# Performance work log

Hardware: AMD Instinct MI355X
Metric: run time of the kernel (lower is better)

## Reference

```python
import jax, jax.numpy as jnp
import numpy as np
from jax import lax

D_MODEL = 1024; N_HEADS = 16; D_FF = 4096
D_INNER = 2048; D_STATE = 16; D_CONV = 4; DT_RANK = 64
B = 4; T = 1024; TF = 512
HD = D_MODEL // N_HEADS


def setup_inputs() -> dict:
    key = jax.random.key(0)
    ks = jax.random.split(key, 24)
    r = lambda i, shape, s=0.02: jax.random.normal(ks[i], shape, jnp.float32) * s
    lengths = jnp.array([512, 384, 448, 320])
    styled_mask = jnp.arange(TF)[None, :] < lengths[:, None]  # True = valid
    inp = {
        'x': jax.random.normal(ks[0], (B, T, D_MODEL), jnp.float32),
        'styled_frames': jax.random.normal(ks[1], (B, TF, D_MODEL), jnp.float32),
        'styled_mask': styled_mask,
        'ln1_g': jnp.ones((D_MODEL,)), 'ln1_b': jnp.zeros((D_MODEL,)),
        'ln2_g': jnp.ones((D_MODEL,)), 'ln2_b': jnp.zeros((D_MODEL,)),
        'ln3_g': jnp.ones((D_MODEL,)), 'ln3_b': jnp.zeros((D_MODEL,)),
        'm_in_w': r(2, (D_MODEL, 2 * D_INNER)),
        'm_conv_w': r(3, (D_INNER, D_CONV), 0.1),
        'm_conv_b': jnp.zeros((D_INNER,)),
        'm_xproj_w': r(4, (D_INNER, DT_RANK + 2 * D_STATE)),
        'm_dt_w': r(5, (DT_RANK, D_INNER), 0.1),
        'm_dt_b': jnp.full((D_INNER,), -4.6),  # softplus -> dt ~ 0.01
        'm_A_log': jnp.log(jnp.broadcast_to(jnp.arange(1, D_STATE + 1, dtype=jnp.float32), (D_INNER, D_STATE))),
        'm_D': jnp.ones((D_INNER,)),
        'm_out_w': r(6, (D_INNER, D_MODEL)),
        'attn_in_w': r(7, (3 * D_MODEL, D_MODEL)),
        'attn_in_b': jnp.zeros((3 * D_MODEL,)),
        'attn_out_w': r(8, (D_MODEL, D_MODEL)),
        'attn_out_b': jnp.zeros((D_MODEL,)),
        'ff_w1': r(9, (D_MODEL, D_FF)),
        'ff_b1': jnp.zeros((D_FF,)),
        'ff_w2': r(10, (D_FF, D_MODEL)),
        'ff_b2': jnp.zeros((D_MODEL,)),
    }
    return inp


def _layer_norm(x, g, b):
    m = x.mean(-1, keepdims=True)
    v = ((x - m) ** 2).mean(-1, keepdims=True)
    return (x - m) / jnp.sqrt(v + 1e-5) * g + b


def _mamba(h, m_in_w, m_conv_w, m_conv_b, m_xproj_w, m_dt_w, m_dt_b, m_A_log, m_D, m_out_w):
    xz = h @ m_in_w                                   # (B,T,2*d_inner)
    xm, z = jnp.split(xz, 2, axis=-1)
    # causal depthwise conv1d
    xt = jnp.pad(xm.transpose(0, 2, 1), ((0, 0), (0, 0), (D_CONV - 1, 0)))  # (B,d_inner,T+pad)
    xc = lax.conv_general_dilated(xt, m_conv_w[:, None, :], (1,), 'VALID',
                                  feature_group_count=D_INNER,
                                  dimension_numbers=('NCH', 'OIH', 'NCH'))
    xc = jax.nn.silu(xc + m_conv_b[None, :, None]).transpose(0, 2, 1)       # (B,T,d_inner)
    x_dbl = xc @ m_xproj_w
    dt, Bs, Cs = jnp.split(x_dbl, [DT_RANK, DT_RANK + D_STATE], axis=-1)
    dt = jax.nn.softplus(dt @ m_dt_w + m_dt_b)        # (B,T,d_inner)
    A = -jnp.exp(m_A_log)                             # (d_inner,d_state)

    def step(hs, inp):
        dt_t, B_t, C_t, u_t = inp                     # (B,d_inner),(B,d_state),(B,d_state),(B,d_inner)
        dA = jnp.exp(dt_t[:, :, None] * A)            # (B,d_inner,d_state)
        hs = dA * hs + dt_t[:, :, None] * B_t[:, None, :] * u_t[:, :, None]
        y = jnp.einsum('bds,bs->bd', hs, C_t)
        return hs, y

    h0 = jnp.zeros((xc.shape[0], D_INNER, D_STATE), xc.dtype)
    inputs = (dt.transpose(1, 0, 2), Bs.transpose(1, 0, 2), Cs.transpose(1, 0, 2), xc.transpose(1, 0, 2))
    hT, ys = lax.scan(step, h0, inputs)
    y = ys.transpose(1, 0, 2) + xc * m_D
    y = y * jax.nn.silu(z)
    return y @ m_out_w, hT


def _cross_attn(q_in, kv_in, valid_mask, in_w, in_b, out_w, out_b):
    d = D_MODEL
    q = q_in @ in_w[:d].T + in_b[:d]
    k = kv_in @ in_w[d:2 * d].T + in_b[d:2 * d]
    v = kv_in @ in_w[2 * d:].T + in_b[2 * d:]
    q = q.reshape(q.shape[0], q.shape[1], N_HEADS, HD)
    k = k.reshape(k.shape[0], k.shape[1], N_HEADS, HD)
    v = v.reshape(v.shape[0], v.shape[1], N_HEADS, HD)
    scores = jnp.einsum('bqhd,bkhd->bhqk', q, k) / np.sqrt(HD)
    scores = jnp.where(valid_mask[:, None, None, :], scores, jnp.finfo(scores.dtype).min)
    attn = jax.nn.softmax(scores, axis=-1)
    o = jnp.einsum('bhqk,bkhd->bqhd', attn, v).reshape(q_in.shape)
    return o @ out_w.T + out_b


def reference(x, styled_frames, styled_mask,
              ln1_g, ln1_b, ln2_g, ln2_b, ln3_g, ln3_b,
              m_in_w, m_conv_w, m_conv_b, m_xproj_w, m_dt_w, m_dt_b, m_A_log, m_D, m_out_w,
              attn_in_w, attn_in_b, attn_out_w, attn_out_b,
              ff_w1, ff_b1, ff_w2, ff_b2):
    h = _layer_norm(x, ln1_g, ln1_b)
    h_mamba, new_state = _mamba(h, m_in_w, m_conv_w, m_conv_b, m_xproj_w, m_dt_w, m_dt_b, m_A_log, m_D, m_out_w)
    x = x + h_mamba
    h = _layer_norm(x, ln2_g, ln2_b)
    x = x + _cross_attn(h, styled_frames, styled_mask, attn_in_w, attn_in_b, attn_out_w, attn_out_b)
    h = _layer_norm(x, ln3_g, ln3_b)
    ff = jax.nn.gelu(h @ ff_w1 + ff_b1, approximate=False) @ ff_w2 + ff_b2
    x = x + ff
    return x, new_state
```

## Files before the change

kernel.cpp:

```cpp
#include <hip/hip_runtime.h>
#include <hip/hip_bf16.h>
#include <cstdint>

using bf16 = __hip_bfloat16;

typedef __attribute__((ext_vector_type(8))) short short8;
typedef __attribute__((ext_vector_type(4))) float floatx4;

__device__ __forceinline__ float b2f(bf16 h) { return __bfloat162float(h); }
__device__ __forceinline__ bf16 f2b(float f) { return __float2bfloat16(f); }
__device__ __forceinline__ float uitf(unsigned u) { union { unsigned u; float f; } c; c.u = u; return c.f; }

__device__ __forceinline__ void async16(const bf16* g, bf16* l) {
    __builtin_amdgcn_global_load_lds(
        (const __attribute__((address_space(1))) uint32_t*)(const void*)g,
        (__attribute__((address_space(3))) uint32_t*)(void*)l, 16, 0, 0);
}

__global__ void lens_flag_kernel(const unsigned char* __restrict__ mask,
                                 const unsigned int* __restrict__ ln1g_raw,
                                 int* __restrict__ hdr) {
    __shared__ int cnt[4];
    int tid = threadIdx.x;
    if (tid < 4) cnt[tid] = 0;
    __syncthreads();
    unsigned char b0 = mask[0], b1 = mask[1];
    int width = (b1 == 0) ? 4 : ((b0 == 1) ? 1 : 2);
    if (width == 4) {
        const unsigned int* m = (const unsigned int*)mask;
        for (int i = tid; i < 2048; i += 256) if (m[i] != 0u) atomicAdd(&cnt[i >> 9], 1);
    } else if (width == 2) {
        const unsigned short* m = (const unsigned short*)mask;
        for (int i = tid; i < 2048; i += 256) if (m[i] != 0u) atomicAdd(&cnt[i >> 9], 1);
    } else {
        for (int i = tid; i < 2048; i += 256) if (mask[i] != 0u) atomicAdd(&cnt[i >> 9], 1);
    }
    __syncthreads();
    if (tid < 4) hdr[tid] = cnt[tid];
    if (tid == 4) hdr[4] = (ln1g_raw[0] == 0x3F800000u) ? 1 : 0;
}

__global__ void convert_kernel(const void* __restrict__ src, bf16* __restrict__ dst, int n,
                               const int* __restrict__ flagp) {
    int i = blockIdx.x * 256 + threadIdx.x;
    if (i >= n) return;
    if (*flagp) dst[i] = f2b(((const float*)src)[i]);
    else        dst[i] = ((const bf16*)src)[i];
}

struct SmallSrcs { const void* p[15]; };
__global__ void convert_smalls_kernel(SmallSrcs s, bf16* __restrict__ dst,
                                      const int* __restrict__ flagp) {
    const int ends[16] = {0, 1024, 2048, 3072, 4096, 5120, 6144, 14336, 16384, 18432,
                          51200, 53248, 56320, 57344, 61440, 62464};
    int i = blockIdx.x * 256 + threadIdx.x;
    if (i >= 62464) return;
    int seg = 0;
    #pragma unroll
    for (int k = 1; k < 16; ++k) if (i >= ends[k]) seg = k;
    int local = i - ends[seg];
    const void* sp = s.p[seg];
    if (*flagp) dst[i] = f2b(((const float*)sp)[local]);
    else        dst[i] = ((const bf16*)sp)[local];
}

__global__ void transpose_any(const void* __restrict__ src, bf16* __restrict__ dst,
                              int R, int C, const int* __restrict__ flagp) {
    __shared__ bf16 tile[32][33];
    bool f32 = (*flagp != 0);
    int bx = blockIdx.x * 32, by = blockIdx.y * 32;
    int tx = threadIdx.x;
    for (int i = threadIdx.y; i < 32; i += 8) {
        int y = by + i, x = bx + tx;
        if (y < R && x < C) {
            size_t idx = (size_t)y * C + x;
            tile[i][tx] = f32 ? f2b(((const float*)src)[idx]) : ((const bf16*)src)[idx];
        }
    }
    __syncthreads();
    for (int i = threadIdx.y; i < 32; i += 8) {
        int yo = bx + i, xo = by + tx;
        if (yo < C && xo < R) dst[(size_t)yo * R + xo] = tile[tx][i];
    }
}

__global__ void vtrans_kernel(const bf16* __restrict__ kv, bf16* __restrict__ vt) {
    __shared__ bf16 t[32][33];
    int kc = blockIdx.x * 32, dc = blockIdx.y * 32;
    int bh = blockIdx.z; int b = bh >> 4, h = bh & 15;
    int tx = threadIdx.x;
    for (int i = threadIdx.y; i < 32; i += 8)
        t[i][tx] = kv[(size_t)(b * 512 + kc + i) * 2048 + 1024 + h * 64 + dc + tx];
    __syncthreads();
    for (int i = threadIdx.y; i < 32; i += 8)
        vt[(size_t)(bh * 64 + dc + i) * 512 + kc + tx] = t[tx][i];
}

__global__ __launch_bounds__(256) void ln_kernel(const bf16* __restrict__ x, const bf16* __restrict__ g,
                                                 const bf16* __restrict__ bb, bf16* __restrict__ out) {
    int row = blockIdx.x, tid = threadIdx.x;
    const bf16* xr = x + (size_t)row * 1024;
    float v[4];
    {
        uint2 raw = *(const uint2*)(xr + tid * 4);
        v[0] = uitf(raw.x << 16); v[1] = uitf(raw.x & 0xffff0000u);
        v[2] = uitf(raw.y << 16); v[3] = uitf(raw.y & 0xffff0000u);
    }
    float sum = v[0] + v[1] + v[2] + v[3];
    float sq = v[0]*v[0] + v[1]*v[1] + v[2]*v[2] + v[3]*v[3];
    for (int off = 32; off; off >>= 1) { sum += __shfl_xor(sum, off); sq += __shfl_xor(sq, off); }
    __shared__ float wsm[8];
    int wave = tid >> 6;
    if ((tid & 63) == 0) { wsm[wave * 2] = sum; wsm[wave * 2 + 1] = sq; }
    __syncthreads();
    sum = wsm[0] + wsm[2] + wsm[4] + wsm[6];
    sq  = wsm[1] + wsm[3] + wsm[5] + wsm[7];
    float mean = sum * (1.f / 1024.f);
    float var = sq * (1.f / 1024.f) - mean * mean;
    float rstd = rsqrtf(var + 1e-5f);
    bf16* orow = out + (size_t)row * 1024;
    #pragma unroll
    for (int c = 0; c < 4; ++c) {
        int col = tid * 4 + c;
        orow[col] = f2b((v[c] - mean) * rstd * b2f(g[col]) + b2f(bb[col]));
    }
}

template<int BN>
__global__ __launch_bounds__(256) void gemm_bt(
    const bf16* __restrict__ A, int lda,
    const bf16* __restrict__ Bt, int ldb,
    void* __restrict__ Cp, int ldc, int c_f32,
    int M, int N, int K,
    const bf16* __restrict__ bias,
    const bf16* __restrict__ res, int ldres,
    int act)
{
    constexpr int NJ = BN / 32;
    __shared__ __align__(16) bf16 As[3][128 * 32];
    __shared__ __align__(16) bf16 Bs[3][BN * 32];
    const int tid = threadIdx.x;
    const int lane = tid & 63;
    const int wave = tid >> 6;
    const int wr = (wave >> 1) * 64;
    const int wc = (wave & 1) * (BN / 2);
    const int lrow = lane & 15;
    const int quad = lane >> 4;

    const int gx = gridDim.x;
    const int nwg = gx * gridDim.y;
    const int orig = blockIdx.y * gx + blockIdx.x;
    int wgid = orig;
    if ((nwg & 7) == 0) wgid = (orig & 7) * (nwg >> 3) + (orig >> 3);
    const int n0 = (wgid % gx) * BN;
    const int m0 = (wgid / gx) * 128;

    const int r0 = tid >> 2;
    const int c0 = (((tid & 3) ^ ((r0 >> 1) & 3)) << 3);

    floatx4 acc[4][NJ];
    #pragma unroll
    for (int i = 0; i < 4; ++i)
        #pragma unroll
        for (int j = 0; j < NJ; ++j) acc[i][j] = (floatx4){0.f, 0.f, 0.f, 0.f};

    const int n1 = n0 + r0, n2 = n0 + r0 + 64;
    const bool fullN = (n0 + BN <= N);
    const bool bok1 = n1 < N, bok2 = n2 < N;
    const int4 z4 = {0, 0, 0, 0};

    const bf16* Ag1 = A + (size_t)(m0 + r0) * lda + c0;
    const bf16* Ag2 = A + (size_t)(m0 + r0 + 64) * lda + c0;
    const bf16* Bg1 = Bt + (size_t)n1 * ldb + c0;
    const bf16* Bg2 = Bt + (size_t)n2 * ldb + c0;

    const int chsw = ((quad ^ ((lrow >> 1) & 3)) << 3);
    const int nt = K >> 5;

    if (fullN) {
        auto stage = [&](int buf, int k0) {
            bf16* AsW = &As[buf][tid * 8];
            bf16* BsW = &Bs[buf][tid * 8];
            async16(Ag1 + k0, AsW);
            async16(Ag2 + k0, AsW + 64 * 32);
            async16(Bg1 + k0, BsW);
            if constexpr (BN == 128) async16(Bg2 + k0, BsW + 64 * 32);
        };
        stage(0, 0);
        if (nt > 1) stage(1, 32);
        int cur = 0;
        for (int t = 0; t < nt; ++t) {
            if (t + 1 < nt) {
                if constexpr (BN == 128) asm volatile("s_waitcnt vmcnt(4)" ::: "memory");
                else                     asm volatile("s_waitcnt vmcnt(3)" ::: "memory");
            } else {
                asm volatile("s_waitcnt vmcnt(0)" ::: "memory");
            }
            __builtin_amdgcn_s_barrier();
            __builtin_amdgcn_sched_barrier(0);
            if (t + 2 < nt) {
                int nb = cur + 2; if (nb >= 3) nb -= 3;
                stage(nb, (t + 2) << 5);
            }
            short8 af[4], bfr[NJ];
            #pragma unroll
            for (int i = 0; i < 4; ++i) af[i]  = *(const short8*)&As[cur][(wr + i * 16 + lrow) * 32 + chsw];
            #pragma unroll
            for (int j = 0; j < NJ; ++j) bfr[j] = *(const short8*)&Bs[cur][(wc + j * 16 + lrow) * 32 + chsw];
            #pragma unroll
            for (int i = 0; i < 4; ++i)
                #pragma unroll
                for (int j = 0; j < NJ; ++j)
                    acc[i][j] = __builtin_amdgcn_mfma_f32_16x16x32_bf16(bfr[j], af[i], acc[i][j], 0, 0, 0);
            if (++cur == 3) cur = 0;
        }
    } else {
        bf16* AsW = &As[0][tid * 8];
        bf16* BsW = &Bs[0][tid * 8];
        for (int k0 = 0; k0 < K; k0 += 32) {
            __syncthreads();
            async16(Ag1 + k0, AsW);
            async16(Ag2 + k0, AsW + 64 * 32);
            *(int4*)BsW = bok1 ? *(const int4*)(Bg1 + k0) : z4;
            if constexpr (BN == 128)
                *(int4*)(BsW + 64 * 32) = bok2 ? *(const int4*)(Bg2 + k0) : z4;
            __syncthreads();
            short8 af[4], bfr[NJ];
            #pragma unroll
            for (int i = 0; i < 4; ++i) af[i]  = *(const short8*)&As[0][(wr + i * 16 + lrow) * 32 + chsw];
            #pragma unroll
            for (int j = 0; j < NJ; ++j) bfr[j] = *(const short8*)&Bs[0][(wc + j * 16 + lrow) * 32 + chsw];
            #pragma unroll
            for (int i = 0; i < 4; ++i)
                #pragma unroll
                for (int j = 0; j < NJ; ++j)
                    acc[i][j] = __builtin_amdgcn_mfma_f32_16x16x32_bf16(bfr[j], af[i], acc[i][j], 0, 0, 0);
        }
    }

    #pragma unroll
    for (int i = 0; i < 4; ++i) {
        const int row = m0 + wr + i * 16 + lrow;
        #pragma unroll
        for (int j = 0; j < NJ; ++j) {
            const int col = n0 + wc + j * 16 + quad * 4;
            float v4[4];
            #pragma unroll
            for (int r = 0; r < 4; ++r) {
                float v = acc[i][j][r];
                if (bias) v += b2f(bias[col + r]);
                if (act == 1)      v = 0.5f * v * (1.f + erff(v * 0.70710678118f));
                else if (act == 2) v = (v > 15.f) ? v : log1pf(__expf(v));
                v4[r] = v;
            }
            if (col + 4 <= N) {
                if (res) {
                    uint2 rr = *(const uint2*)(res + (size_t)row * ldres + col);
                    v4[0] += uitf(rr.x << 16); v4[1] += uitf(rr.x & 0xffff0000u);
                    v4[2] += uitf(rr.y << 16); v4[3] += uitf(rr.y & 0xffff0000u);
                }
                if (c_f32) {
                    float4 o = {v4[0], v4[1], v4[2], v4[3]};
                    *(float4*)((float*)Cp + (size_t)row * ldc + col) = o;
                } else {
                    bf16 o[4] = {f2b(v4[0]), f2b(v4[1]), f2b(v4[2]), f2b(v4[3])};
                    *(uint2*)((bf16*)Cp + (size_t)row * ldc + col) = *(uint2*)o;
                }
            } else {
                #pragma unroll
                for (int r = 0; r < 4; ++r) {
                    if (col + r >= N) continue;
                    float v = v4[r];
                    if (res) v += b2f(res[(size_t)row * ldres + col + r]);
                    if (c_f32) ((float*)Cp)[(size_t)row * ldc + col + r] = v;
                    else       ((bf16*)Cp)[(size_t)row * ldc + col + r] = f2b(v);
                }
            }
        }
    }
}

__global__ __launch_bounds__(512) void gemm_bt_big(
    const bf16* __restrict__ A, int lda,
    const bf16* __restrict__ Bt, int ldb,
    void* __restrict__ Cp, int ldc, int c_f32,
    int M, int N, int K,
    const bf16* __restrict__ bias,
    const bf16* __restrict__ res, int ldres,
    int act)
{
    __shared__ __align__(16) bf16 As[3][256 * 32];
    __shared__ __align__(16) bf16 Bs[3][256 * 32];
    const int tid = threadIdx.x;
    const int lane = tid & 63;
    const int wave = tid >> 6;
    const int wm = wave >> 2;
    const int wn = wave & 3;
    const int lrow = lane & 15;
    const int quad = lane >> 4;

    const int gx = gridDim.x;
    const int nwg = gx * gridDim.y;
    const int orig = blockIdx.y * gx + blockIdx.x;
    int wgid = orig;
    if ((nwg & 7) == 0) wgid = (orig & 7) * (nwg >> 3) + (orig >> 3);
    const int n0 = (wgid % gx) * 256;
    const int m0 = (wgid / gx) * 256;

    const int r0 = tid >> 2;
    const int c0 = (((tid & 3) ^ ((r0 >> 1) & 3)) << 3);

    floatx4 acc[8][4];
    #pragma unroll
    for (int i = 0; i < 8; ++i)
        #pragma unroll
        for (int j = 0; j < 4; ++j) acc[i][j] = (floatx4){0.f, 0.f, 0.f, 0.f};

    const bf16* Ag1 = A + (size_t)(m0 + r0) * lda + c0;
    const bf16* Ag2 = A + (size_t)(m0 + r0 + 128) * lda + c0;
    const bf16* Bg1 = Bt + (size_t)(n0 + r0) * ldb + c0;
    const bf16* Bg2 = Bt + (size_t)(n0 + r0 + 128) * ldb + c0;

    const int chsw = ((quad ^ ((lrow >> 1) & 3)) << 3);
    const int nt = K >> 5;

    auto stage = [&](int buf, int k0) {
        bf16* AsW = &As[buf][tid * 8];
        bf16* BsW = &Bs[buf][tid * 8];
        async16(Ag1 + k0, AsW);
        async16(Ag2 + k0, AsW + 128 * 32);
        async16(Bg1 + k0, BsW);
        async16(Bg2 + k0, BsW + 128 * 32);
    };
    stage(0, 0);
    stage(1, 32);
    int cur = 0;
    for (int t = 0; t < nt; ++t) {
        if (t + 1 < nt) asm volatile("s_waitcnt vmcnt(4)" ::: "memory");
        else            asm volatile("s_waitcnt vmcnt(0)" ::: "memory");
        __builtin_amdgcn_s_barrier();
        __builtin_amdgcn_sched_barrier(0);
        if (t + 2 < nt) {
            int nb = cur + 2; if (nb >= 3) nb -= 3;
            stage(nb, (t + 2) << 5);
        }
        short8 af[8], bfr[4];
        #pragma unroll
        for (int i = 0; i < 8; ++i)
            af[i] = *(const short8*)&As[cur][(wm * 128 + i * 16 + lrow) * 32 + chsw];
        #pragma unroll
        for (int j = 0; j < 4; ++j)
            bfr[j] = *(const short8*)&Bs[cur][(wn * 64 + j * 16 + lrow) * 32 + chsw];
        #pragma unroll
        for (int i = 0; i < 8; ++i)
            #pragma unroll
            for (int j = 0; j < 4; ++j)
                acc[i][j] = __builtin_amdgcn_mfma_f32_16x16x32_bf16(bfr[j], af[i], acc[i][j], 0, 0, 0);
        if (++cur == 3) cur = 0;
    }

    #pragma unroll
    for (int i = 0; i < 8; ++i) {
        const int row = m0 + wm * 128 + i * 16 + lrow;
        #pragma unroll
        for (int j = 0; j < 4; ++j) {
            const int col = n0 + wn * 64 + j * 16 + quad * 4;
            float v4[4];
            #pragma unroll
            for (int r = 0; r < 4; ++r) {
                float v = acc[i][j][r];
                if (bias) v += b2f(bias[col + r]);
                if (act == 1)      v = 0.5f * v * (1.f + erff(v * 0.70710678118f));
                else if (act == 2) v = (v > 15.f) ? v : log1pf(__expf(v));
                v4[r] = v;
            }
            if (res) {
                uint2 rr = *(const uint2*)(res + (size_t)row * ldres + col);
                v4[0] += uitf(rr.x << 16); v4[1] += uitf(rr.x & 0xffff0000u);
                v4[2] += uitf(rr.y << 16); v4[3] += uitf(rr.y & 0xffff0000u);
            }
            if (c_f32) {
                float4 o = {v4[0], v4[1], v4[2], v4[3]};
                *(float4*)((float*)Cp + (size_t)row * ldc + col) = o;
            } else {
                bf16 o[4] = {f2b(v4[0]), f2b(v4[1]), f2b(v4[2]), f2b(v4[3])};
                *(uint2*)((bf16*)Cp + (size_t)row * ldc + col) = *(uint2*)o;
            }
        }
    }
}

__global__ __launch_bounds__(256) void conv_silu_kernel(const bf16* __restrict__ xz, const bf16* __restrict__ cw,
                                                        const bf16* __restrict__ cb, bf16* __restrict__ xc) {
    int idx = blockIdx.x * 256 + threadIdx.x;
    int d = idx & 2047;
    int row = idx >> 11;
    int t = row & 1023;
    int base = row - t;
    float acc = b2f(cb[d]);
    #pragma unroll
    for (int j = 0; j < 4; ++j) {
        int tt = t - 3 + j;
        if (tt >= 0) acc += b2f(xz[(size_t)(base + tt) * 4096 + d]) * b2f(cw[d * 4 + j]);
    }
    xc[idx] = f2b(acc * (1.f / (1.f + __expf(-acc))));
}

__global__ __launch_bounds__(256) void scan_part1(
    const bf16* __restrict__ dt, const bf16* __restrict__ xc, const bf16* __restrict__ xdbl,
    const bf16* __restrict__ A_log, float* __restrict__ Pb, float* __restrict__ qb)
{
    __shared__ float smB[128][20];
    const int tid = threadIdx.x;
    const int dgrp = blockIdx.x, c = blockIdx.y, b = blockIdx.z;
    const int dl = tid >> 1, sh = tid & 1;
    const int d = (dgrp << 7) + dl;
    const size_t rowbase = (size_t)b * 1024 + (size_t)c * 128;

    {
        int r = tid >> 1, q = tid & 1;
        short8 raw = *(const short8*)(xdbl + (rowbase + r) * 96 + 64 + q * 8);
        #pragma unroll
        for (int j = 0; j < 8; ++j) smB[r][q * 8 + j] = b2f(((const bf16*)&raw)[j]);
    }
    __syncthreads();

    float A2[8], h[8];
    #pragma unroll
    for (int s = 0; s < 8; ++s) {
        A2[s] = -__expf(b2f(A_log[d * 16 + sh * 8 + s])) * 1.44269504f;
        h[s] = 0.f;
    }
    float dtsum = 0.f;
    const bf16* dtp = dt + rowbase * 2048 + d;
    const bf16* up  = xc + rowbase * 2048 + d;
    for (int tc = 0; tc < 128; tc += 8) {
        float dtv[8], uv[8];
        #pragma unroll
        for (int i = 0; i < 8; ++i) {
            dtv[i] = b2f(dtp[(size_t)(tc + i) * 2048]);
            uv[i]  = b2f(up[(size_t)(tc + i) * 2048]);
        }
        #pragma unroll
        for (int i = 0; i < 8; ++i) {
            float dtf = dtv[i];
            dtsum += dtf;
            float w = dtf * uv[i];
            float4 B0 = *(const float4*)&smB[tc + i][sh * 8];
            float4 B1 = *(const float4*)&smB[tc + i][sh * 8 + 4];
            float Bv[8] = {B0.x, B0.y, B0.z, B0.w, B1.x, B1.y, B1.z, B1.w};
            #pragma unroll
            for (int s = 0; s < 8; ++s) {
                float e = __builtin_amdgcn_exp2f(dtf * A2[s]);
                h[s] = fmaf(e, h[s], w * Bv[s]);
            }
        }
    }
    size_t gid = ((size_t)(b * 2048 + d) * 16 + sh * 8) + (size_t)c * 131072;
    float Pv[8];
    #pragma unroll
    for (int s = 0; s < 8; ++s) Pv[s] = __builtin_amdgcn_exp2f(A2[s] * dtsum);
    *(float4*)(Pb + gid)     = *(float4*)&Pv[0];
    *(float4*)(Pb + gid + 4) = *(float4*)&Pv[4];
    *(float4*)(qb + gid)     = *(float4*)&h[0];
    *(float4*)(qb + gid + 4) = *(float4*)&h[4];
}

__global__ __launch_bounds__(256) void scan_stitch(
    const float* __restrict__ Pb, const float* __restrict__ qb,
    float* __restrict__ hs, float* __restrict__ state_out)
{
    int gid = blockIdx.x * 256 + threadIdx.x;
    float h = 0.f;
    #pragma unroll
    for (int c = 0; c < 8; ++c) {
        hs[gid + c * 131072] = h;
        h = Pb[gid + c * 131072] * h + qb[gid + c * 131072];
    }
    state_out[gid] = h;
}

__global__ __launch_bounds__(256) void scan_part3(
    const bf16* __restrict__ dt, const bf16* __restrict__ xc, const bf16* __restrict__ xdbl,
    const bf16* __restrict__ xz, const bf16* __restrict__ A_log, const bf16* __restrict__ Dp,
    const float* __restrict__ hs, bf16* __restrict__ ymul)
{
    __shared__ float smBC[128][36];
    const int tid = threadIdx.x;
    const int dgrp = blockIdx.x, c = blockIdx.y, b = blockIdx.z;
    const int dl = tid >> 1, sh = tid & 1;
    const int d = (dgrp << 7) + dl;
    const size_t rowbase = (size_t)b * 1024 + (size_t)c * 128;

    {
        int r = tid >> 1, q = tid & 1;
        const bf16* src = xdbl + (rowbase + r) * 96 + 64 + q * 16;
        short8 raw0 = *(const short8*)src;
        short8 raw1 = *(const short8*)(src + 8);
        #pragma unroll
        for (int j = 0; j < 8; ++j) {
            smBC[r][q * 16 + j]     = b2f(((const bf16*)&raw0)[j]);
            smBC[r][q * 16 + 8 + j] = b2f(((const bf16*)&raw1)[j]);
        }
    }
    __syncthreads();

    float A2[8], h[8];
    size_t gid = ((size_t)(b * 2048 + d) * 16 + sh * 8) + (size_t)c * 131072;
    {
        float4 h0 = *(const float4*)(hs + gid);
        float4 h1 = *(const float4*)(hs + gid + 4);
        h[0] = h0.x; h[1] = h0.y; h[2] = h0.z; h[3] = h0.w;
        h[4] = h1.x; h[5] = h1.y; h[6] = h1.z; h[7] = h1.w;
    }
    #pragma unroll
    for (int s = 0; s < 8; ++s)
        A2[s] = -__expf(b2f(A_log[d * 16 + sh * 8 + s])) * 1.44269504f;
    const float Dv = b2f(Dp[d]);
    const bf16* dtp = dt + rowbase * 2048 + d;
    const bf16* up  = xc + rowbase * 2048 + d;
    const bf16* zp  = xz + rowbase * 4096 + 2048 + d;
    bf16* yp = ymul + rowbase * 2048 + d;
    for (int tc = 0; tc < 128; tc += 8) {
        float dtv[8], uv[8], zv[8];
        #pragma unroll
        for (int i = 0; i < 8; ++i) {
            dtv[i] = b2f(dtp[(size_t)(tc + i) * 2048]);
            uv[i]  = b2f(up[(size_t)(tc + i) * 2048]);
            zv[i]  = b2f(zp[(size_t)(tc + i) * 4096]);
        }
        #pragma unroll
        for (int i = 0; i < 8; ++i) {
            float dtf = dtv[i], uf = uv[i];
            float w = dtf * uf;
            float4 B0 = *(const float4*)&smBC[tc + i][sh * 8];
            float4 B1 = *(const float4*)&smBC[tc + i][sh * 8 + 4];
            float4 C0 = *(const float4*)&smBC[tc + i][16 + sh * 8];
            float4 C1 = *(const float4*)&smBC[tc + i][16 + sh * 8 + 4];
            float Bv[8] = {B0.x, B0.y, B0.z, B0.w, B1.x, B1.y, B1.z, B1.w};
            float Cv[8] = {C0.x, C0.y, C0.z, C0.w, C1.x, C1.y, C1.z, C1.w};
            float y = 0.f;
            #pragma unroll
            for (int s = 0; s < 8; ++s) {
                float e = __builtin_amdgcn_exp2f(dtf * A2[s]);
                h[s] = fmaf(e, h[s], w * Bv[s]);
                y = fmaf(h[s], Cv[s], y);
            }
            y += __shfl_xor(y, 1);
            float z = zv[i];
            float sig = __builtin_amdgcn_rcpf(1.f + __builtin_amdgcn_exp2f(-1.44269504f * z));
            float o = (y + uf * Dv) * (z * sig);
            if (sh == 0) yp[(size_t)(tc + i) * 2048] = f2b(o);
        }
    }
}

__global__ __launch_bounds__(256) void attn_mfma(
    const bf16* __restrict__ qb, const bf16* __restrict__ kv, const bf16* __restrict__ vt,
    const int* __restrict__ lens, bf16* __restrict__ ob)
{
    const int qt = blockIdx.x, h = blockIdx.y, b = blockIdx.z;
    const int tid = threadIdx.x;
    const int wave = tid >> 6;
    const int lane = tid & 63;
    const int l15 = lane & 15;
    const int quad = lane >> 4;
    const int len = lens[b];

    __shared__ __align__(16) bf16 Ps[32][520];
    __shared__ float red_sh[4][32];

    short8 aq[2][2];
    const bf16* qbase = qb + (size_t)(b * 1024 + qt * 32 + l15) * 1024 + h * 64 + quad * 8;
    #pragma unroll
    for (int mt = 0; mt < 2; ++mt)
        #pragma unroll
        for (int ks = 0; ks < 2; ++ks)
            aq[mt][ks] = *(const short8*)(qbase + (size_t)mt * 16 * 1024 + ks * 32);

    floatx4 accs[2][8];
    #pragma unroll
    for (int mt = 0; mt < 2; ++mt)
        #pragma unroll
        for (int nt = 0; nt < 8; ++nt) accs[mt][nt] = (floatx4){0.f, 0.f, 0.f, 0.f};

    const bf16* kbase = kv + (size_t)(b * 512 + wave * 128 + l15) * 2048 + h * 64 + quad * 8;
    #pragma unroll
    for (int nt = 0; nt < 8; ++nt) {
        short8 bk0 = *(const short8*)(kbase + (size_t)nt * 16 * 2048);
        short8 bk1 = *(const short8*)(kbase + (size_t)nt * 16 * 2048 + 32);
        #pragma unroll
        for (int mt = 0; mt < 2; ++mt) {
            accs[mt][nt] = __builtin_amdgcn_mfma_f32_16x16x32_bf16(aq[mt][0], bk0, accs[mt][nt], 0, 0, 0);
            accs[mt][nt] = __builtin_amdgcn_mfma_f32_16x16x32_bf16(aq[mt][1], bk1, accs[mt][nt], 0, 0, 0);
        }
    }

    float pm[2][4];
    #pragma unroll
    for (int mt = 0; mt < 2; ++mt)
        #pragma unroll
        for (int r = 0; r < 4; ++r) pm[mt][r] = -1e30f;
    #pragma unroll
    for (int mt = 0; mt < 2; ++mt)
        #pragma unroll
        for (int nt = 0; nt < 8; ++nt) {
            int col = wave * 128 + nt * 16 + l15;
            bool ok = col < len;
            #pragma unroll
            for (int r = 0; r < 4; ++r) {
                float s = ok ? accs[mt][nt][r] * 0.125f : -1e30f;
                accs[mt][nt][r] = s;
                pm[mt][r] = fmaxf(pm[mt][r], s);
            }
        }
    #pragma unroll
    for (int off = 1; off < 16; off <<= 1)
        #pragma unroll
        for (int mt = 0; mt < 2; ++mt)
            #pragma unroll
            for (int r = 0; r < 4; ++r) pm[mt][r] = fmaxf(pm[mt][r], __shfl_xor(pm[mt][r], off));
    if (l15 == 0)
        #pragma unroll
        for (int mt = 0; mt < 2; ++mt)
            #pragma unroll
            for (int r = 0; r < 4; ++r) red_sh[wave][mt * 16 + quad * 4 + r] = pm[mt][r];
    __syncthreads();
    float rowmax[2][4];
    #pragma unroll
    for (int mt = 0; mt < 2; ++mt)
        #pragma unroll
        for (int r = 0; r < 4; ++r) {
            int row = mt * 16 + quad * 4 + r;
            rowmax[mt][r] = fmaxf(fmaxf(red_sh[0][row], red_sh[1][row]),
                                  fmaxf(red_sh[2][row], red_sh[3][row]));
        }
    __syncthreads();

    float ps[2][4] = {{0.f, 0.f, 0.f, 0.f}, {0.f, 0.f, 0.f, 0.f}};
    #pragma unroll
    for (int mt = 0; mt < 2; ++mt)
        #pragma unroll
        for (int nt = 0; nt < 8; ++nt)
            #pragma unroll
            for (int r = 0; r < 4; ++r) {
                float p = __expf(accs[mt][nt][r] - rowmax[mt][r]);
                accs[mt][nt][r] = p;
                ps[mt][r] += p;
            }
    #pragma unroll
    for (int off = 1; off < 16; off <<= 1)
        #pragma unroll
        for (int mt = 0; mt < 2; ++mt)
            #pragma unroll
            for (int r = 0; r < 4; ++r) ps[mt][r] += __shfl_xor(ps[mt][r], off);
    if (l15 == 0)
        #pragma unroll
        for (int mt = 0; mt < 2; ++mt)
            #pragma unroll
            for (int r = 0; r < 4; ++r) red_sh[wave][mt * 16 + quad * 4 + r] = ps[mt][r];
    #pragma unroll
    for (int mt = 0; mt < 2; ++mt)
        #pragma unroll
        for (int nt = 0; nt < 8; ++nt)
            #pragma unroll
            for (int r = 0; r < 4; ++r)
                Ps[mt * 16 + quad * 4 + r][wave * 128 + nt * 16 + l15] = f2b(accs[mt][nt][r]);
    __syncthreads();
    float rowsum[2][4];
    #pragma unroll
    for (int mt = 0; mt < 2; ++mt)
        #pragma unroll
        for (int r = 0; r < 4; ++r) {
            int row = mt * 16 + quad * 4 + r;
            rowsum[mt][r] = red_sh[0][row] + red_sh[1][row] + red_sh[2][row] + red_sh[3][row];
        }

    floatx4 acco[2];
    acco[0] = (floatx4){0.f, 0.f, 0.f, 0.f};
    acco[1] = (floatx4){0.f, 0.f, 0.f, 0.f};
    const bf16* vtbase = vt + (size_t)((b * 16 + h) * 64 + wave * 16 + l15) * 512 + quad * 8;
    #pragma unroll
    for (int kc = 0; kc < 16; ++kc) {
        short8 bv = *(const short8*)(vtbase + kc * 32);
        short8 ap0 = *(const short8*)&Ps[l15][kc * 32 + quad * 8];
        short8 ap1 = *(const short8*)&Ps[16 + l15][kc * 32 + quad * 8];
        acco[0] = __builtin_amdgcn_mfma_f32_16x16x32_bf16(ap0, bv, acco[0], 0, 0, 0);
        acco[1] = __builtin_amdgcn_mfma_f32_16x16x32_bf16(ap1, bv, acco[1], 0, 0, 0);
    }

    #pragma unroll
    for (int mt = 0; mt < 2; ++mt)
        #pragma unroll
        for (int r = 0; r < 4; ++r) {
            int row = b * 1024 + qt * 32 + mt * 16 + quad * 4 + r;
            int col = h * 64 + wave * 16 + l15;
            ob[(size_t)row * 1024 + col] = f2b(acco[mt][r] / rowsum[mt][r]);
        }
}

extern "C" void kernel_launch(void* const* d_in, const int* in_sizes, int n_in,
                              void* d_out, int out_size, void* d_ws, size_t ws_size,
                              hipStream_t stream) {
    bf16* W = (bf16*)d_ws;
    int* hdr = (int*)d_ws;
    const int* flagp = hdr + 4;
    const size_t CV_X     = 32;
    const size_t CV_ST    = CV_X    + 4194304;
    const size_t CV_AIW   = CV_ST   + 2097152;
    const size_t CV_AOW   = CV_AIW  + 3145728;
    const size_t CV_SM    = CV_AOW  + 1048576;
    const size_t WT_IN    = CV_SM   + 62464;
    const size_t WT_XPROJ = WT_IN   + 4194304;
    const size_t WT_DT    = WT_XPROJ + 196608;
    const size_t WT_OUT   = WT_DT   + 131072;
    const size_t WT_FF1   = WT_OUT  + 2097152;
    const size_t WT_FF2   = WT_FF1  + 4194304;
    const size_t HB   = WT_FF2 + 4194304;
    const size_t XZ   = HB     + 4194304;
    const size_t XC   = XZ     + 16777216;
    const size_t XDBL = XC     + 8388608;
    const size_t DTB  = XDBL   + 393216;
    const size_t YM   = DTB    + 8388608;
    const size_t X2  = HB;
    const size_t HB2 = DTB;
    const size_t Qb  = XZ;
    const size_t KV  = XZ + 4194304;
    const size_t AO  = XC;
    const size_t VT  = XC + 4194304;
    const size_t X3  = YM;
    const size_t HB3 = DTB;
    const size_t FFH = XZ;
    float* Pb = (float*)(W + HB);
    float* qbuf = Pb + 1048576;
    float* hstart = (float*)(W + WT_IN);
    const size_t S_LN1G = 0, S_LN1B = 1024, S_LN2G = 2048, S_LN2B = 3072, S_LN3G = 4096, S_LN3B = 5120;
    const size_t S_CW = 6144, S_CB = 14336, S_DTB = 16384, S_AL = 18432, S_D = 51200;
    const size_t S_AIB = 53248, S_AOB = 56320, S_FB1 = 57344, S_FB2 = 61440;

    float* out = (float*)d_out;
    float* state_out = out + (size_t)4 * 1024 * 1024;

    lens_flag_kernel<<<1, 256, 0, stream>>>((const unsigned char*)d_in[2],
                                            (const unsigned int*)d_in[3], hdr);
    convert_kernel<<<16384, 256, 0, stream>>>(d_in[0],  W + CV_X,   4194304, flagp);
    convert_kernel<<<8192,  256, 0, stream>>>(d_in[1],  W + CV_ST,  2097152, flagp);
    convert_kernel<<<12288, 256, 0, stream>>>(d_in[18], W + CV_AIW, 3145728, flagp);
    convert_kernel<<<4096,  256, 0, stream>>>(d_in[20], W + CV_AOW, 1048576, flagp);
    SmallSrcs ss;
    ss.p[0] = d_in[3];  ss.p[1] = d_in[4];  ss.p[2] = d_in[5];  ss.p[3] = d_in[6];
    ss.p[4] = d_in[7];  ss.p[5] = d_in[8];  ss.p[6] = d_in[10]; ss.p[7] = d_in[11];
    ss.p[8] = d_in[14]; ss.p[9] = d_in[15]; ss.p[10] = d_in[16]; ss.p[11] = d_in[19];
    ss.p[12] = d_in[21]; ss.p[13] = d_in[23]; ss.p[14] = d_in[25];
    convert_smalls_kernel<<<245, 256, 0, stream>>>(ss, W + CV_SM, flagp);

    dim3 tb(32, 8);
    transpose_any<<<dim3(128, 32), tb, 0, stream>>>(d_in[9],  W + WT_IN,    1024, 4096, flagp);
    transpose_any<<<dim3(3, 64),   tb, 0, stream>>>(d_in[12], W + WT_XPROJ, 2048, 96,   flagp);
    transpose_any<<<dim3(64, 2),   tb, 0, stream>>>(d_in[13], W + WT_DT,    64,   2048, flagp);
    transpose_any<<<dim3(32, 64),  tb, 0, stream>>>(d_in[17], W + WT_OUT,   2048, 1024, flagp);
    transpose_any<<<dim3(128, 32), tb, 0, stream>>>(d_in[22], W + WT_FF1,   1024, 4096, flagp);
    transpose_any<<<dim3(32, 128), tb, 0, stream>>>(d_in[24], W + WT_FF2,   4096, 1024, flagp);

    auto gemm = [&](const bf16* A, int lda, const bf16* Bt, int ldb, void* C, int ldc, int c_f32,
                    int M, int N, int K, const bf16* bias, const bf16* res, int ldres, int act) {
        if (M >= 4096 && N >= 4096 && (M & 255) == 0 && (N & 255) == 0 && (K & 31) == 0 && K >= 64) {
            dim3 grid(N / 256, M / 256);
            gemm_bt_big<<<grid, 512, 0, stream>>>(A, lda, Bt, ldb, C, ldc, c_f32, M, N, K, bias, res, ldres, act);
        } else if ((N & 127) == 0 && N <= 2048) {
            dim3 grid(N / 64, M / 128);
            gemm_bt<64><<<grid, 256, 0, stream>>>(A, lda, Bt, ldb, C, ldc, c_f32, M, N, K, bias, res, ldres, act);
        } else {
            dim3 grid((N + 127) / 128, M / 128);
            gemm_bt<128><<<grid, 256, 0, stream>>>(A, lda, Bt, ldb, C, ldc, c_f32, M, N, K, bias, res, ldres, act);
        }
    };

    ln_kernel<<<4096, 256, 0, stream>>>(W + CV_X, W + CV_SM + S_LN1G, W + CV_SM + S_LN1B, W + HB);
    gemm(W + HB, 1024, W + WT_IN, 1024, W + XZ, 4096, 0, 4096, 4096, 1024, nullptr, nullptr, 0, 0);
    conv_silu_kernel<<<32768, 256, 0, stream>>>(W + XZ, W + CV_SM + S_CW, W + CV_SM + S_CB, W + XC);
    gemm(W + XC, 2048, W + WT_XPROJ, 2048, W + XDBL, 96, 0, 4096, 96, 2048, nullptr, nullptr, 0, 0);
    gemm(W + XDBL, 96, W + WT_DT, 64, W + DTB, 2048, 0, 4096, 2048, 64, W + CV_SM + S_DTB, nullptr, 0, 2);
    scan_part1<<<dim3(16, 8, 4), 256, 0, stream>>>(W + DTB, W + XC, W + XDBL, W + CV_SM + S_AL, Pb, qbuf);
    scan_stitch<<<512, 256, 0, stream>>>(Pb, qbuf, hstart, state_out);
    scan_part3<<<dim3(16, 8, 4), 256, 0, stream>>>(W + DTB, W + XC, W + XDBL, W + XZ,
                                                   W + CV_SM + S_AL, W + CV_SM + S_D, hstart, W + YM);
    gemm(W + YM, 2048, W + WT_OUT, 2048, W + X2, 1024, 0, 4096, 1024, 2048, nullptr, W + CV_X, 1024, 0);

    ln_kernel<<<4096, 256, 0, stream>>>(W + X2, W + CV_SM + S_LN2G, W + CV_SM + S_LN2B, W + HB2);
    gemm(W + HB2, 1024, W + CV_AIW, 1024, W + Qb, 1024, 0, 4096, 1024, 1024, W + CV_SM + S_AIB, nullptr, 0, 0);
    gemm(W + CV_ST, 1024, W + CV_AIW + 1048576, 1024, W + KV, 2048, 0, 2048, 2048, 1024, W + CV_SM + S_AIB + 1024, nullptr, 0, 0);
    vtrans_kernel<<<dim3(16, 2, 64), tb, 0, stream>>>(W + KV, W + VT);
    attn_mfma<<<dim3(32, 16, 4), 256, 0, stream>>>(W + Qb, W + KV, W + VT, hdr, W + AO);
    gemm(W + AO, 1024, W + CV_AOW, 1024, W + X3, 1024, 0, 4096, 1024, 1024, W + CV_SM + S_AOB, W + X2, 1024, 0);

    ln_kernel<<<4096, 256, 0, stream>>>(W + X3, W + CV_SM + S_LN3G, W + CV_SM + S_LN3B, W + HB3);
    gemm(W + HB3, 1024, W + WT_FF1, 1024, W + FFH, 4096, 0, 4096, 4096, 1024, W + CV_SM + S_FB1, nullptr, 0, 1);
    gemm(W + FFH, 4096, W + WT_FF2, 4096, out, 1024, 1, 4096, 1024, 4096, W + CV_SM + S_FB2, W + X3, 1024, 0);
}
```

Before: 929.2 us.

## Restructure big GEMM into double-buffered K=64 tiles with phased load/MFMA interleave

The large 256x256 GEMM moves from a triple-buffered K=32 pipeline to a double-buffered K=64 pipeline. Each K step is split into four phases that interleave fragment loads, MFMA groups and the async global-to-LDS staging of the next tile. The phases are fenced with barriers and partial vmcnt waits, and s_setprio raises priority around the MFMA blocks. The aim is better overlap of memory and matrix work and fewer barriers per unit of K, at the cost of more barriers per iteration and a larger LDS footprint (128KB total).

```diff
diff --git a/kernel.cpp b/kernel.cpp
--- a/kernel.cpp
+++ b/kernel.cpp
@@ -280,7 +280,7 @@
     }
 }
 
-__global__ __launch_bounds__(512) void gemm_bt_big(
+__global__ __launch_bounds__(512) void gemm_8ph(
     const bf16* __restrict__ A, int lda,
     const bf16* __restrict__ Bt, int ldb,
     void* __restrict__ Cp, int ldc, int c_f32,
@@ -289,8 +289,8 @@
     const bf16* __restrict__ res, int ldres,
     int act)
 {
-    __shared__ __align__(16) bf16 As[3][256 * 32];
-    __shared__ __align__(16) bf16 Bs[3][256 * 32];
+    __shared__ __align__(16) bf16 As[2][256 * 64];
+    __shared__ __align__(16) bf16 Bs[2][256 * 64];
     const int tid = threadIdx.x;
     const int lane = tid & 63;
     const int wave = tid >> 6;
@@ -307,8 +307,10 @@
     const int n0 = (wgid % gx) * 256;
     const int m0 = (wgid / gx) * 256;
 
-    const int r0 = tid >> 2;
-    const int c0 = (((tid & 3) ^ ((r0 >> 1) & 3)) << 3);
+    const int srow = tid >> 3;
+    const int scol = (((tid & 7) ^ ((tid >> 3) & 7)) << 3);
+    const bf16* Ag = A + (size_t)(m0 + srow) * lda + scol;
+    const bf16* Bg = Bt + (size_t)(n0 + srow) * ldb + scol;
 
     floatx4 acc[8][4];
     #pragma unroll
@@ -316,47 +318,73 @@
         #pragma unroll
         for (int j = 0; j < 4; ++j) acc[i][j] = (floatx4){0.f, 0.f, 0.f, 0.f};
 
-    const bf16* Ag1 = A + (size_t)(m0 + r0) * lda + c0;
-    const bf16* Ag2 = A + (size_t)(m0 + r0 + 128) * lda + c0;
-    const bf16* Bg1 = Bt + (size_t)(n0 + r0) * ldb + c0;
-    const bf16* Bg2 = Bt + (size_t)(n0 + r0 + 128) * ldb + c0;
-
-    const int chsw = ((quad ^ ((lrow >> 1) & 3)) << 3);
-    const int nt = K >> 5;
-
-    auto stage = [&](int buf, int k0) {
-        bf16* AsW = &As[buf][tid * 8];
-        bf16* BsW = &Bs[buf][tid * 8];
-        async16(Ag1 + k0, AsW);
-        async16(Ag2 + k0, AsW + 128 * 32);
-        async16(Bg1 + k0, BsW);
-        async16(Bg2 + k0, BsW + 128 * 32);
+    auto stageA = [&](int buf, int k0, int u) {
+        async16(Ag + (size_t)(u * 64) * lda + k0, &As[buf][u * 4096 + tid * 8]);
     };
-    stage(0, 0);
-    stage(1, 32);
-    int cur = 0;
+    auto stageB = [&](int buf, int k0, int u) {
+        async16(Bg + (size_t)(u * 64) * ldb + k0, &Bs[buf][u * 4096 + tid * 8]);
+    };
+
+    const int nt = K >> 6;
+    stageB(0, 0, 0); stageB(0, 0, 1);
+    stageB(0, 0, 2); stageB(0, 0, 3);
+    stageA(0, 0, 0); stageA(0, 0, 2);
+    stageA(0, 0, 1); stageA(0, 0, 3);
+    asm volatile("s_waitcnt vmcnt(2)" ::: "memory");
+    __builtin_amdgcn_s_barrier();
+    __builtin_amdgcn_sched_barrier(0);
+
+    const int csw = lrow & 7;
+
     for (int t = 0; t < nt; ++t) {
-        if (t + 1 < nt) asm volatile("s_waitcnt vmcnt(4)" ::: "memory");
-        else            asm volatile("s_waitcnt vmcnt(0)" ::: "memory");
-        __builtin_amdgcn_s_barrier();
-        __builtin_amdgcn_sched_barrier(0);
-        if (t + 2 < nt) {
-            int nb = cur + 2; if (nb >= 3) nb -= 3;
-            stage(nb, (t + 2) << 5);
-        }
-        short8 af[8], bfr[4];
-        #pragma unroll
-        for (int i = 0; i < 8; ++i)
-            af[i] = *(const short8*)&As[cur][(wm * 128 + i * 16 + lrow) * 32 + chsw];
-        #pragma unroll
-        for (int j = 0; j < 4; ++j)
-            bfr[j] = *(const short8*)&Bs[cur][(wn * 64 + j * 16 + lrow) * 32 + chsw];
-        #pragma unroll
-        for (int i = 0; i < 8; ++i)
-            #pragma unroll
-            for (int j = 0; j < 4; ++j)
-                acc[i][j] = __builtin_amdgcn_mfma_f32_16x16x32_bf16(bfr[j], af[i], acc[i][j], 0, 0, 0);
-        if (++cur == 3) cur = 0;
+        const int cur = t & 1, nb = cur ^ 1;
+        const bool more = (t + 1) < nt;
+        const int k1 = (t + 1) << 6;
+        short8 bfr[4][2];
+        #pragma unroll
+        for (int p = 0; p < 4; ++p) {
+            short8 af[2][2];
+            #pragma unroll
+            for (int e = 0; e < 2; ++e)
+                #pragma unroll
+                for (int k = 0; k < 2; ++k)
+                    af[e][k] = *(const short8*)&As[cur][(wm * 128 + (2 * p + e) * 16 + lrow) * 64
+                                                       + (((k * 4 + quad) ^ csw) << 3)];
+            if (p == 0) {
+                #pragma unroll
+                for (int nf = 0; nf < 4; ++nf)
+                    #pragma unroll
+                    for (int k = 0; k < 2; ++k)
+                        bfr[nf][k] = *(const short8*)&Bs[cur][(wn * 64 + nf * 16 + lrow) * 64
+                                                             + (((k * 4 + quad) ^ csw) << 3)];
+            }
+            if (more) {
+                if (p == 0)      { stageB(nb, k1, 0); stageB(nb, k1, 1); }
+                else if (p == 1) { stageB(nb, k1, 2); stageB(nb, k1, 3); }
+                else if (p == 2) { stageA(nb, k1, 0); stageA(nb, k1, 2); }
+                else             { stageA(nb, k1, 1); stageA(nb, k1, 3); }
+            }
+            __builtin_amdgcn_s_setprio(1);
+            #pragma unroll
+            for (int e = 0; e < 2; ++e)
+                #pragma unroll
+                for (int nf = 0; nf < 4; ++nf)
+                    #pragma unroll
+                    for (int k = 0; k < 2; ++k)
+                        acc[2 * p + e][nf] = __builtin_amdgcn_mfma_f32_16x16x32_bf16(
+                            bfr[nf][k], af[e][k], acc[2 * p + e][nf], 0, 0, 0);
+            __builtin_amdgcn_s_setprio(0);
+            if (p == 1) {
+                if (more) asm volatile("s_waitcnt vmcnt(4)" ::: "memory");
+                else      asm volatile("s_waitcnt vmcnt(0)" ::: "memory");
+            }
+            if (p == 3 && more)
+                asm volatile("s_waitcnt vmcnt(2)" ::: "memory");
+            if (p < 3 || more) {
+                __builtin_amdgcn_s_barrier();
+                __builtin_amdgcn_sched_barrier(0);
+            }
+        }
     }
 
     #pragma unroll
@@ -764,9 +792,9 @@
 
     auto gemm = [&](const bf16* A, int lda, const bf16* Bt, int ldb, void* C, int ldc, int c_f32,
                     int M, int N, int K, const bf16* bias, const bf16* res, int ldres, int act) {
-        if (M >= 4096 && N >= 4096 && (M & 255) == 0 && (N & 255) == 0 && (K & 31) == 0 && K >= 64) {
+        if (M >= 4096 && N >= 4096 && (M & 255) == 0 && (N & 255) == 0 && (K & 63) == 0) {
             dim3 grid(N / 256, M / 256);
-            gemm_bt_big<<<grid, 512, 0, stream>>>(A, lda, Bt, ldb, C, ldc, c_f32, M, N, K, bias, res, ldres, act);
+            gemm_8ph<<<grid, 512, 0, stream>>>(A, lda, Bt, ldb, C, ldc, c_f32, M, N, K, bias, res, ldres, act);
         } else if ((N & 127) == 0 && N <= 2048) {
             dim3 grid(N / 64, M / 128);
             gemm_bt<64><<<grid, 256, 0, stream>>>(A, lda, Bt, ldb, C, ldc, c_f32, M, N, K, bias, res, ldres, act);
```

Result: no change. 940.4 us (+1.2%).
